# Performance work log

Measured on AMD Instinct MI355X. Metric: run time of the kernel, lower is better.

## Reference

```python
import jax, jax.numpy as jnp
import numpy as np

HIDDEN = 1280
NUM_HEADS = 16
NUM_KV_HEADS = 4
HEAD_DIM = 80
Q_SIZE = NUM_HEADS * HEAD_DIM          # 1280
KV_SIZE = NUM_KV_HEADS * HEAD_DIM      # 320
QKV_OUT = Q_SIZE + 2 * KV_SIZE         # 1920
R_SOFTPLUS_0 = 1.442695041


def setup_inputs() -> dict:
    key = jax.random.key(0)
    ks = jax.random.split(key, 6)
    B, S = 4, 2048
    return {
        "hidden_states": jax.random.normal(ks[0], (B, S, HIDDEN), dtype=jnp.float32),
        "scaling": jax.random.normal(ks[1], (HEAD_DIM,), dtype=jnp.float32),
        "qkv_w": jax.random.normal(ks[2], (QKV_OUT, HIDDEN), dtype=jnp.float32) * (1.0 / np.sqrt(HIDDEN)),
        "qkv_b": jax.random.normal(ks[3], (QKV_OUT,), dtype=jnp.float32) * 0.01,
        "o_w": jax.random.normal(ks[4], (HIDDEN, Q_SIZE), dtype=jnp.float32) * (1.0 / np.sqrt(Q_SIZE)),
        "o_b": jax.random.normal(ks[5], (HIDDEN,), dtype=jnp.float32) * 0.01,
    }


def reference(hidden_states, scaling, qkv_w, qkv_b, o_w, o_b):
    B, S, _ = hidden_states.shape
    qkv = hidden_states @ qkv_w.T + qkv_b                      # [B,S,1920]
    xq = qkv[..., :Q_SIZE].reshape(B, S, NUM_HEADS, HEAD_DIM)
    xk = qkv[..., Q_SIZE:Q_SIZE + KV_SIZE].reshape(B, S, NUM_KV_HEADS, HEAD_DIM)
    xv = qkv[..., Q_SIZE + KV_SIZE:].reshape(B, S, NUM_KV_HEADS, HEAD_DIM)
    # learned per-head-dim scaling: (r_softplus_0/sqrt(d)) * softplus(scaling)
    scale = (R_SOFTPLUS_0 / np.sqrt(HEAD_DIM)) * jax.nn.softplus(scaling)
    xq = xq * scale[None, None, None, :]
    # GQA: expand kv heads to match query heads (repeat_interleave on head dim)
    nq_per_kv = NUM_HEADS // NUM_KV_HEADS
    k = jnp.repeat(xk, nq_per_kv, axis=2)                      # [B,S,H,d]
    v = jnp.repeat(xv, nq_per_kv, axis=2)
    scores = jnp.einsum("bqhd,bkhd->bhqk", xq, k)              # [B,H,S,S]
    probs = jax.nn.softmax(scores.astype(jnp.float32), axis=-1).astype(xq.dtype)
    out = jnp.einsum("bhqk,bkhd->bqhd", probs, v)              # [B,S,H,d]
    out = out.reshape(B, S, Q_SIZE)
    return out @ o_w.T + o_b
```

## Files before the change

kernel.cpp:

```cpp
#include <hip/hip_runtime.h>

#define HIDDEN 1280
#define QOUT   1920
#define QSIZE  1280
#define KVSIZE 320
#define NHEAD  16
#define NKV    4
#define DH     80
#define SEQ    2048
#define BATCH  4
#define MTOT   (BATCH * SEQ)
#define NT64   (SEQ / 64)
#define KTILE_ELEMS 6144
#define VTILE_ELEMS 5120

typedef __attribute__((ext_vector_type(8))) short bf16x8;
typedef __attribute__((ext_vector_type(4))) short bf16x4;
typedef __attribute__((ext_vector_type(4))) float f32x4;

__device__ __forceinline__ unsigned short f2bf(float x) {
  union { float f; unsigned u; } v; v.f = x;
  unsigned r = v.u + 0x7fffu + ((v.u >> 16) & 1u);
  return (unsigned short)(r >> 16);
}

__device__ __forceinline__ unsigned packbf(float a, float b) {
  union { float f; unsigned u; } ua, ub;
  ua.f = a; ub.f = b;
  return __builtin_amdgcn_perm(ub.u + 0x8000u, ua.u + 0x8000u, 0x07060302u);
}

__device__ __forceinline__ unsigned packbf_t(float a, float b) {
  union { float f; unsigned u; } ua, ub;
  ua.f = a; ub.f = b;
  return __builtin_amdgcn_perm(ub.u, ua.u, 0x07060302u);
}

__device__ __forceinline__ float exp2x(float x) {
#if __has_builtin(__builtin_amdgcn_exp2f)
  return __builtin_amdgcn_exp2f(x);
#else
  return exp2f(x);
#endif
}

__device__ __forceinline__ void async_copy16(const void* g, void* lds) {
  __builtin_amdgcn_global_load_lds(
      (const __attribute__((address_space(1))) unsigned int*)g,
      (__attribute__((address_space(3))) unsigned int*)lds, 16, 0, 0);
}

#define HSB   (MTOT * HIDDEN / 4 / 256)
#define QWB   (QOUT * HIDDEN / 4 / 256)
#define OWB   (HIDDEN * QSIZE / 4 / 256)
__global__ __launch_bounds__(256) void prep_k(const float* __restrict__ hs,
                                              const float* __restrict__ qkv_w,
                                              const float* __restrict__ o_w,
                                              const float* __restrict__ scaling,
                                              unsigned short* __restrict__ hs_bf,
                                              unsigned short* __restrict__ qkvw_bf,
                                              unsigned short* __restrict__ ow_bf,
                                              float* __restrict__ cs) {
  const int bid = blockIdx.x, tid = threadIdx.x;
  const float* src; unsigned short* dst; int i;
  if (bid < HSB)            { src = hs;    dst = hs_bf;   i = bid * 256 + tid; }
  else if (bid < HSB + QWB) { src = qkv_w; dst = qkvw_bf; i = (bid - HSB) * 256 + tid; }
  else if (bid < HSB + QWB + OWB) { src = o_w; dst = ow_bf; i = (bid - HSB - QWB) * 256 + tid; }
  else {
    int n = (bid - HSB - QWB - OWB) * 256 + tid;
    if (n < QOUT) {
      float v = 1.0f;
      if (n < QSIZE) {
        float x = scaling[n % DH];
        float sp = (x > 20.f) ? x : log1pf(__expf(x));
        v = 1.442695041f * 1.442695041f * 0.11180339887f * sp;
      }
      cs[n] = v;
    }
    return;
  }
  float4 v = ((const float4*)src)[i];
  ushort4 o;
  o.x = f2bf(v.x); o.y = f2bf(v.y); o.z = f2bf(v.z); o.w = f2bf(v.w);
  ((ushort4*)dst)[i] = o;
}

template <bool OUT_BF16, bool USE_SCALE>
__global__ __launch_bounds__(512) void gemm_bt(const unsigned short* __restrict__ A,
                                               const unsigned short* __restrict__ Bt,
                                               const float* __restrict__ bias,
                                               const float* __restrict__ colscale,
                                               void* __restrict__ Cout,
                                               int M, int N, int K) {
  __shared__ unsigned short As[256 * 64];
  __shared__ unsigned short Bs[128 * 64];
  const int tid  = threadIdx.x;
  const int wave = tid >> 6, lane = tid & 63;
  const int r = lane & 15, quad = lane >> 4;
  const int xm = r & 7;
  const int m0 = blockIdx.y * 256, n0 = blockIdx.x * 128;
  const int rm = (wave >> 1) * 64, cn = (wave & 1) * 64;

  f32x4 acc[4][4];
#pragma unroll
  for (int i = 0; i < 4; ++i)
#pragma unroll
    for (int j = 0; j < 4; ++j) acc[i][j] = f32x4{0.f, 0.f, 0.f, 0.f};

  for (int k0 = 0; k0 < K; k0 += 64) {
    __syncthreads();
#pragma unroll
    for (int j = 0; j < 4; ++j) {
      const int c = tid + j * 512;
      const int row = c >> 3, sp = c & 7;
      const int sd = (sp ^ (row & 7)) * 8;
      async_copy16(A + (size_t)(m0 + row) * K + k0 + sd, &As[c * 8]);
    }
#pragma unroll
    for (int j = 0; j < 2; ++j) {
      const int c = tid + j * 512;
      const int row = c >> 3, sp = c & 7;
      const int sd = (sp ^ (row & 7)) * 8;
      async_copy16(Bt + (size_t)(n0 + row) * K + k0 + sd, &Bs[c * 8]);
    }
    __syncthreads();
#pragma unroll
    for (int kk = 0; kk < 2; ++kk) {
      bf16x8 af[4], bfr[4];
#pragma unroll
      for (int mi = 0; mi < 4; ++mi)
        af[mi] = *(const bf16x8*)&As[(rm + mi * 16 + r) * 64 + ((kk * 4 + quad) ^ xm) * 8];
#pragma unroll
      for (int ni = 0; ni < 4; ++ni)
        bfr[ni] = *(const bf16x8*)&Bs[(cn + ni * 16 + r) * 64 + ((kk * 4 + quad) ^ xm) * 8];
#pragma unroll
      for (int mi = 0; mi < 4; ++mi)
#pragma unroll
        for (int ni = 0; ni < 4; ++ni)
          acc[mi][ni] = __builtin_amdgcn_mfma_f32_16x16x32_bf16(af[mi], bfr[ni], acc[mi][ni], 0, 0, 0);
    }
  }

#pragma unroll
  for (int ni = 0; ni < 4; ++ni) {
    const int n = n0 + cn + ni * 16 + r;
    const float bn = bias[n];
    const float sc = USE_SCALE ? colscale[n] : 1.0f;
#pragma unroll
    for (int mi = 0; mi < 4; ++mi) {
#pragma unroll
      for (int reg = 0; reg < 4; ++reg) {
        const int m = m0 + rm + mi * 16 + quad * 4 + reg;
        const float v = (acc[mi][ni][reg] + bn) * sc;
        if (OUT_BF16)
          ((unsigned short*)Cout)[(size_t)m * N + n] = f2bf(v);
        else
          ((float*)Cout)[(size_t)m * N + n] = v;
      }
    }
  }
}

__global__ __launch_bounds__(256) void kvpack(const unsigned short* __restrict__ qkv,
                                              unsigned short* __restrict__ Kp,
                                              unsigned short* __restrict__ Vp) {
  const int st = blockIdx.x, kvh = blockIdx.y, b = blockIdx.z;
  const int tid = threadIdx.x;
  unsigned short* kout = Kp + (size_t)((b * NKV + kvh) * NT64 + st) * KTILE_ELEMS;
#pragma unroll
  for (int j = 0; j < 3; ++j) {
    int c = tid + j * 256;
    int row = c / 12, cir = c - row * 12;
    int kk = cir >> 2, sp = cir & 3;
    int sd = sp ^ ((row >> 1) & 3);
    int d0 = kk * 32 + sd * 8;
    int skey = (row >> 5) * 32 + ((row >> 2) & 3) * 8 + ((row >> 4) & 1) * 4 + (row & 3);
    uint4 v = {0, 0, 0, 0};
    if (d0 < DH)
      v = *(const uint4*)&qkv[(size_t)(b * SEQ + st * 64 + skey) * QOUT +
                              QSIZE + kvh * DH + d0];
    *(uint4*)&kout[row * 96 + kk * 32 + sp * 8] = v;
  }
  __shared__ unsigned short tile[64][88];
  for (int c = tid; c < 640; c += 256) {
    int row = c / 10, seg = c % 10;
    uint4 v = *(const uint4*)&qkv[(size_t)(b * SEQ + st * 64 + row) * QOUT +
                                  QSIZE + KVSIZE + kvh * DH + seg * 8];
    *(uint4*)&tile[row][seg * 8] = v;
  }
  __syncthreads();
  unsigned short* vout = Vp + (size_t)((b * NKV + kvh) * NT64 + st) * VTILE_ELEMS;
  for (int c = tid; c < 5120; c += 256) {
    int d = c >> 6, key = c & 63;
    vout[d * 64 + (key ^ ((d & 7) << 3))] = tile[key][d];
  }
}

__global__ __launch_bounds__(512, 4) void attn(const unsigned short* __restrict__ qkv,
                                               const unsigned short* __restrict__ Kp,
                                               const unsigned short* __restrict__ Vp,
                                               unsigned short* __restrict__ att) {
  const int qt = blockIdx.x, h = blockIdx.y, b = blockIdx.z;
  const int kvh = h >> 2;
  const int tid = threadIdx.x;
  const int wave = tid >> 6, lane = tid & 63;
  const int r = lane & 15, quad = lane >> 4;
  const int sq8 = (quad ^ ((r >> 1) & 3)) * 8;

  __shared__ unsigned short Ks[2][64 * 96];
  __shared__ unsigned short Vs[2][96 * 64];

  {
    const uint4 ones = {0x3F803F80u, 0x3F803F80u, 0x3F803F80u, 0x3F803F80u};
    for (int c = tid; c < 256; c += 512)
      *(uint4*)&Vs[c >> 7][80 * 64 + (c & 127) * 8] = ones;
  }

  const int qbase = qt * 256 + wave * 32;
  bf16x8 qb[2][3];
#pragma unroll
  for (int t = 0; t < 2; ++t)
#pragma unroll
    for (int kk = 0; kk < 3; ++kk)
      qb[t][kk] = *(const bf16x8*)&qkv[(size_t)(b * SEQ + qbase + t * 16 + r) * QOUT +
                                       h * DH + kk * 32 + quad * 8];

  f32x4 o_acc[6][2];
#pragma unroll
  for (int i = 0; i < 6; ++i)
#pragma unroll
    for (int t = 0; t < 2; ++t) o_acc[i][t] = f32x4{0.f, 0.f, 0.f, 0.f};

  const unsigned short* kp = Kp + (size_t)((b * NKV + kvh) * NT64) * KTILE_ELEMS;
  const unsigned short* vp = Vp + (size_t)((b * NKV + kvh) * NT64) * VTILE_ELEMS;

#define STAGE(bufi, kt_) do {                                                   \
    const unsigned short* kpt = kp + (size_t)(kt_) * KTILE_ELEMS;               \
    async_copy16(kpt + tid * 8, &Ks[bufi][tid * 8]);                            \
    if (tid < 256) async_copy16(kpt + (tid + 512) * 8, &Ks[bufi][(tid + 512) * 8]); \
    const unsigned short* vpt = vp + (size_t)(kt_) * VTILE_ELEMS;               \
    async_copy16(vpt + tid * 8, &Vs[bufi][tid * 8]);                            \
    if (tid < 128) async_copy16(vpt + (tid + 512) * 8, &Vs[bufi][(tid + 512) * 8]); \
  } while (0)

  STAGE(0, 0);
  __syncthreads();

  for (int kt = 0; kt < NT64; ++kt) {
    const int cur = kt & 1;
    if (kt + 1 < NT64) STAGE(cur ^ 1, kt + 1);

#pragma unroll
    for (int ntp = 0; ntp < 2; ++ntp) {
      uint4 pw[2];
      {
        bf16x8 ka[3];
#pragma unroll
        for (int kk = 0; kk < 3; ++kk)
          ka[kk] = *(const bf16x8*)&Ks[cur][(ntp * 32 + r) * 96 + kk * 32 + sq8];
#pragma unroll
        for (int t = 0; t < 2; ++t) {
          f32x4 s = f32x4{0.f, 0.f, 0.f, 0.f};
#pragma unroll
          for (int kk = 0; kk < 3; ++kk)
            s = __builtin_amdgcn_mfma_f32_16x16x32_bf16(ka[kk], qb[t][kk], s, 0, 0, 0);
          pw[t].x = packbf_t(exp2x(s[0]), exp2x(s[1]));
          pw[t].y = packbf_t(exp2x(s[2]), exp2x(s[3]));
        }
      }
      {
        bf16x8 ka[3];
#pragma unroll
        for (int kk = 0; kk < 3; ++kk)
          ka[kk] = *(const bf16x8*)&Ks[cur][(ntp * 32 + 16 + r) * 96 + kk * 32 + sq8];
#pragma unroll
        for (int t = 0; t < 2; ++t) {
          f32x4 s = f32x4{0.f, 0.f, 0.f, 0.f};
#pragma unroll
          for (int kk = 0; kk < 3; ++kk)
            s = __builtin_amdgcn_mfma_f32_16x16x32_bf16(ka[kk], qb[t][kk], s, 0, 0, 0);
          pw[t].z = packbf_t(exp2x(s[0]), exp2x(s[1]));
          pw[t].w = packbf_t(exp2x(s[2]), exp2x(s[3]));
        }
      }

#pragma unroll
      for (int nt2 = 0; nt2 < 6; ++nt2) {
        bf16x8 va = *(const bf16x8*)&Vs[cur][(nt2 * 16 + r) * 64 +
                                             (((ntp * 4 + quad) ^ (r & 7)) << 3)];
#pragma unroll
        for (int t = 0; t < 2; ++t) {
          union { uint4 u; bf16x8 v; } pv; pv.u = pw[t];
          o_acc[nt2][t] = __builtin_amdgcn_mfma_f32_16x16x32_bf16(va, pv.v, o_acc[nt2][t], 0, 0, 0);
        }
      }
    }
    __syncthreads();
  }
#undef STAGE

#pragma unroll
  for (int t = 0; t < 2; ++t) {
    const float il = 1.0f / o_acc[5][t][0];
    const size_t q = (size_t)(b * SEQ + qbase + t * 16 + r);
#pragma unroll
    for (int nt2 = 0; nt2 < 5; ++nt2) {
      uint2 w;
      w.x = packbf(o_acc[nt2][t][0] * il, o_acc[nt2][t][1] * il);
      w.y = packbf(o_acc[nt2][t][2] * il, o_acc[nt2][t][3] * il);
      *(uint2*)&att[q * QSIZE + h * DH + nt2 * 16 + quad * 4] = w;
    }
  }
}

extern "C" void kernel_launch(void* const* d_in, const int* in_sizes, int n_in,
                              void* d_out, int out_size, void* d_ws, size_t ws_size,
                              hipStream_t stream) {
  const float* hs      = (const float*)d_in[0];
  const float* scaling = (const float*)d_in[1];
  const float* qkv_w   = (const float*)d_in[2];
  const float* qkv_b   = (const float*)d_in[3];
  const float* o_w     = (const float*)d_in[4];
  const float* o_b     = (const float*)d_in[5];

  char* p = (char*)d_ws;
  unsigned short* hs_bf   = (unsigned short*)p; p += (size_t)MTOT * HIDDEN * 2;
  unsigned short* qkvw_bf = (unsigned short*)p; p += (size_t)QOUT * HIDDEN * 2;
  unsigned short* ow_bf   = (unsigned short*)p; p += (size_t)HIDDEN * QSIZE * 2;
  float* cscale           = (float*)p;          p += (size_t)QOUT * 4;
  unsigned short* qkv     = (unsigned short*)p; p += (size_t)MTOT * QOUT * 2;
  unsigned short* Kp      = (unsigned short*)p; p += (size_t)BATCH * NKV * NT64 * KTILE_ELEMS * 2;
  unsigned short* Vp      = (unsigned short*)p; p += (size_t)BATCH * NKV * NT64 * VTILE_ELEMS * 2;
  unsigned short* att     = hs_bf;

  prep_k<<<HSB + QWB + OWB + 8, 256, 0, stream>>>(hs, qkv_w, o_w, scaling,
                                                  hs_bf, qkvw_bf, ow_bf, cscale);

  dim3 g1(QOUT / 128, MTOT / 256);
  gemm_bt<true, true><<<g1, 512, 0, stream>>>(hs_bf, qkvw_bf, qkv_b, cscale, qkv,
                                              MTOT, QOUT, HIDDEN);
  dim3 gp(NT64, NKV, BATCH);
  kvpack<<<gp, 256, 0, stream>>>(qkv, Kp, Vp);
  dim3 g3(SEQ / 256, NHEAD, BATCH);
  attn<<<g3, 512, 0, stream>>>(qkv, Kp, Vp, att);
  dim3 g4(QSIZE / 128, MTOT / 256);
  gemm_bt<false, false><<<g4, 512, 0, stream>>>(att, ow_bf, o_b, nullptr, d_out,
                                                MTOT, QSIZE, HIDDEN);
}
```

Before: 278.2 us.

## Swizzle block order for XCD locality and batch QK MFMAs with setprio

Remaps the GEMM and attention block indices so that consecutive blocks are spread in groups of eight, which is meant to place blocks sharing K/V or weight tiles on the same XCD for L2 reuse. Inside the attention loop, all QK^T MFMAs for a 64-key tile are now computed before any exp2, and the MFMA phases are wrapped in s_setprio raises. This is meant to let exp work from one wave overlap with matrix work from other waves. The cost is higher register pressure from holding eight score accumulators, and the attention remap hardcodes the grid shape.

```diff
diff --git a/kernel.cpp b/kernel.cpp
--- a/kernel.cpp
+++ b/kernel.cpp
@@ -98,7 +98,11 @@
   const int wave = tid >> 6, lane = tid & 63;
   const int r = lane & 15, quad = lane >> 4;
   const int xm = r & 7;
-  const int m0 = blockIdx.y * 256, n0 = blockIdx.x * 128;
+  const int gx = gridDim.x;
+  int lid = blockIdx.y * gx + blockIdx.x;
+  const int cpx = (gx * gridDim.y) >> 3;
+  lid = (lid & 7) * cpx + (lid >> 3);
+  const int m0 = (lid / gx) * 256, n0 = (lid % gx) * 128;
   const int rm = (wave >> 1) * 64, cn = (wave & 1) * 64;
 
   f32x4 acc[4][4];
@@ -200,7 +204,12 @@
                                                const unsigned short* __restrict__ Kp,
                                                const unsigned short* __restrict__ Vp,
                                                unsigned short* __restrict__ att) {
-  const int qt = blockIdx.x, h = blockIdx.y, b = blockIdx.z;
+  int qt, h, b;
+  {
+    int lid = (blockIdx.z * 16 + blockIdx.y) * 8 + blockIdx.x;
+    lid = (lid & 7) * 64 + (lid >> 3);
+    qt = lid & 7; h = (lid >> 3) & 15; b = lid >> 7;
+  }
   const int kvh = h >> 2;
   const int tid = threadIdx.x;
   const int wave = tid >> 6, lane = tid & 63;
@@ -250,40 +259,38 @@
     const int cur = kt & 1;
     if (kt + 1 < NT64) STAGE(cur ^ 1, kt + 1);
 
+    f32x4 s[2][2][2];
+    __builtin_amdgcn_s_setprio(1);
+#pragma unroll
+    for (int ntp = 0; ntp < 2; ++ntp)
+#pragma unroll
+      for (int half = 0; half < 2; ++half) {
+        bf16x8 ka[3];
+#pragma unroll
+        for (int kk = 0; kk < 3; ++kk)
+          ka[kk] = *(const bf16x8*)&Ks[cur][(ntp * 32 + half * 16 + r) * 96 + kk * 32 + sq8];
+#pragma unroll
+        for (int t = 0; t < 2; ++t) {
+          f32x4 a0 = f32x4{0.f, 0.f, 0.f, 0.f};
+#pragma unroll
+          for (int kk = 0; kk < 3; ++kk)
+            a0 = __builtin_amdgcn_mfma_f32_16x16x32_bf16(ka[kk], qb[t][kk], a0, 0, 0, 0);
+          s[ntp][half][t] = a0;
+        }
+      }
+    __builtin_amdgcn_s_setprio(0);
+
 #pragma unroll
     for (int ntp = 0; ntp < 2; ++ntp) {
       uint4 pw[2];
-      {
-        bf16x8 ka[3];
-#pragma unroll
-        for (int kk = 0; kk < 3; ++kk)
-          ka[kk] = *(const bf16x8*)&Ks[cur][(ntp * 32 + r) * 96 + kk * 32 + sq8];
-#pragma unroll
-        for (int t = 0; t < 2; ++t) {
-          f32x4 s = f32x4{0.f, 0.f, 0.f, 0.f};
-#pragma unroll
-          for (int kk = 0; kk < 3; ++kk)
-            s = __builtin_amdgcn_mfma_f32_16x16x32_bf16(ka[kk], qb[t][kk], s, 0, 0, 0);
-          pw[t].x = packbf_t(exp2x(s[0]), exp2x(s[1]));
-          pw[t].y = packbf_t(exp2x(s[2]), exp2x(s[3]));
-        }
-      }
-      {
-        bf16x8 ka[3];
-#pragma unroll
-        for (int kk = 0; kk < 3; ++kk)
-          ka[kk] = *(const bf16x8*)&Ks[cur][(ntp * 32 + 16 + r) * 96 + kk * 32 + sq8];
-#pragma unroll
-        for (int t = 0; t < 2; ++t) {
-          f32x4 s = f32x4{0.f, 0.f, 0.f, 0.f};
-#pragma unroll
-          for (int kk = 0; kk < 3; ++kk)
-            s = __builtin_amdgcn_mfma_f32_16x16x32_bf16(ka[kk], qb[t][kk], s, 0, 0, 0);
-          pw[t].z = packbf_t(exp2x(s[0]), exp2x(s[1]));
-          pw[t].w = packbf_t(exp2x(s[2]), exp2x(s[3]));
-        }
-      }
-
+#pragma unroll
+      for (int t = 0; t < 2; ++t) {
+        pw[t].x = packbf_t(exp2x(s[ntp][0][t][0]), exp2x(s[ntp][0][t][1]));
+        pw[t].y = packbf_t(exp2x(s[ntp][0][t][2]), exp2x(s[ntp][0][t][3]));
+        pw[t].z = packbf_t(exp2x(s[ntp][1][t][0]), exp2x(s[ntp][1][t][1]));
+        pw[t].w = packbf_t(exp2x(s[ntp][1][t][2]), exp2x(s[ntp][1][t][3]));
+      }
+      __builtin_amdgcn_s_setprio(1);
 #pragma unroll
       for (int nt2 = 0; nt2 < 6; ++nt2) {
         bf16x8 va = *(const bf16x8*)&Vs[cur][(nt2 * 16 + r) * 64 +
@@ -294,6 +301,7 @@
           o_acc[nt2][t] = __builtin_amdgcn_mfma_f32_16x16x32_bf16(va, pv.v, o_acc[nt2][t], 0, 0, 0);
         }
       }
+      __builtin_amdgcn_s_setprio(0);
     }
     __syncthreads();
   }
```

After: 275.0 us. No clear change (-1.2%).
